# Kernel optimization log

Measured on AMD Instinct MI355X. Metric: run time of the kernel, lower is better.

The kernel has to match this reference:

```python
import jax, jax.numpy as jnp
import numpy as np

N = 50000      # nodes
E = 800000     # directed edges (avg degree 16)
F_IN = 128     # in_channels
HID = 256      # hidden_channels
OUT = 40       # out_channels (classes)


def setup_inputs() -> dict:
    key = jax.random.key(0)
    ks = jax.random.split(key, 6)
    x = jax.random.normal(ks[0], (N, F_IN), dtype=jnp.float32)
    edge_index = jax.random.randint(ks[1], (2, E), 0, N, dtype=jnp.int32)
    W1 = jax.random.normal(ks[2], (F_IN, HID), dtype=jnp.float32) * (1.0 / np.sqrt(F_IN))
    b1 = jnp.zeros((HID,), jnp.float32)
    W2 = jax.random.normal(ks[3], (HID, HID), dtype=jnp.float32) * (1.0 / np.sqrt(HID))
    b2 = jnp.zeros((HID,), jnp.float32)
    Wc = jax.random.normal(ks[4], (HID, OUT), dtype=jnp.float32) * (1.0 / np.sqrt(HID))
    bc = jnp.zeros((OUT,), jnp.float32)
    return {"x": x, "W1": W1, "b1": b1, "W2": W2, "b2": b2,
            "Wc": Wc, "bc": bc, "edge_index": edge_index}


def _gcn_conv(x, W, b, src, dst, norm):
    # PyG GCNConv: linear transform, then normalized sparse aggregation, then bias.
    h = x @ W                                    # [N, H]
    msg = h[src] * norm[:, None]                 # [E+N, H] gather + scale
    agg = jax.ops.segment_sum(msg, dst, num_segments=N)  # scatter-add
    return agg + b


def reference(x, W1, b1, W2, b2, Wc, bc, edge_index):
    # add self-loops (GCNConv default add_self_loops=True)
    loops = jnp.arange(N, dtype=edge_index.dtype)
    src = jnp.concatenate([edge_index[0], loops])
    dst = jnp.concatenate([edge_index[1], loops])
    # symmetric normalization D^-1/2 A D^-1/2 (degree counted at dst)
    deg = jax.ops.segment_sum(jnp.ones_like(dst, dtype=jnp.float32), dst,
                              num_segments=N)
    dinv = jax.lax.rsqrt(jnp.maximum(deg, 1.0))  # deg >= 1 due to self-loops
    norm = dinv[src] * dinv[dst]                 # [E+N]
    # layer 1 + ReLU (dropout is identity in eval mode)
    h = jax.nn.relu(_gcn_conv(x, W1, b1, src, dst, norm))
    # layer 2 + ReLU
    h = jax.nn.relu(_gcn_conv(h, W2, b2, src, dst, norm))
    # dense classifier
    return h @ Wc + bc  # [N, OUT]
```

## Files before the change

kernel.cpp:

```cpp
#include <hip/hip_runtime.h>

#define NNODES 50000
#define NEDGES 800000
#define F_IN   128
#define HID    256
#define NOUT   40
#define NBLK_SCAN ((NNODES + 255) / 256)
#define NBLK_CAST 6250
#define NBLK_DEG  2048
#define NBLK_PREP 432
#define EDGE_CHUNK 3125
#define NODES_PER_G 6250

typedef __attribute__((ext_vector_type(8))) _Float16 f16x8;
typedef __attribute__((ext_vector_type(4))) float f32x4;
typedef __attribute__((ext_vector_type(4))) unsigned short u16x4;
typedef __attribute__((ext_vector_type(8))) unsigned short u16x8;

__device__ __forceinline__ unsigned short f2h(float f) {
  return __builtin_bit_cast(unsigned short, (_Float16)f);
}
__device__ __forceinline__ float h2f(unsigned short u) {
  return (float)__builtin_bit_cast(_Float16, u);
}


__global__ __launch_bounds__(256) void k_pre(const float* __restrict__ X,
                                             unsigned short* __restrict__ Xh,
                                             const int* __restrict__ dst,
                                             int* __restrict__ count,
                                             const float* __restrict__ W1,
                                             const float* __restrict__ W2,
                                             const float* __restrict__ Wc,
                                             unsigned short* __restrict__ T1,
                                             unsigned short* __restrict__ T2,
                                             unsigned short* __restrict__ Tc) {
  int b = blockIdx.x, t = threadIdx.x;
  if (b < NBLK_CAST) {
    int i = b * 256 + t;
    float4 v = *reinterpret_cast<const float4*>(X + (size_t)i * 4);
    ushort4 o;
    o.x = f2h(v.x); o.y = f2h(v.y); o.z = f2h(v.z); o.w = f2h(v.w);
    *reinterpret_cast<ushort4*>(Xh + (size_t)i * 4) = o;
  } else if (b < NBLK_CAST + NBLK_DEG) {
    int db = b - NBLK_CAST;
    int g = b & 7;
    int chunk = db >> 3;
    int lo = g * NODES_PER_G, hi = lo + NODES_PER_G;
    int base = chunk * EDGE_CHUNK;
    for (int i = base + t; i < base + EDGE_CHUNK; i += 256) {
      int d = dst[i];
      if (d >= lo && d < hi) atomicAdd(&count[d], 1);
    }
  } else {
    int pb = b - NBLK_CAST - NBLK_DEG;
    if (pb < 128) {
      int idx = pb * 256 + t;
      int n = idx >> 7, k = idx & 127;
      T1[idx] = f2h(W1[(size_t)k * HID + n]);
    } else if (pb < 384) {
      int idx = (pb - 128) * 256 + t;
      int n = idx >> 8, k = idx & 255;
      T2[idx] = f2h(W2[(size_t)k * HID + n]);
    } else {
      int idx = (pb - 384) * 256 + t;
      int n = idx >> 8, k = idx & 255;
      float v = (n < NOUT) ? Wc[(size_t)k * NOUT + n] : 0.f;
      Tc[idx] = f2h(v);
    }
  }
}


__global__ __launch_bounds__(256) void k_scan1(const int* __restrict__ count,
                                               int* __restrict__ rowstart,
                                               int* __restrict__ bsum,
                                               float* __restrict__ dinv,
                                               int* __restrict__ boff,
                                               int* __restrict__ done) {
  __shared__ int tmp[256];
  __shared__ int lastFlag;
  int t = threadIdx.x;
  int i = blockIdx.x * 256 + t;
  int v = (i < NNODES) ? count[i] : 0;
  if (i < NNODES) dinv[i] = rsqrtf((float)(v + 1));
  tmp[t] = v;
  __syncthreads();
  for (int off = 1; off < 256; off <<= 1) {
    int x = (t >= off) ? tmp[t - off] : 0;
    __syncthreads();
    tmp[t] += x;
    __syncthreads();
  }
  if (i < NNODES) rowstart[i] = tmp[t] - v;
  if (t == 255) {
    bsum[blockIdx.x] = tmp[255];
    __threadfence();
  }
  __syncthreads();
  if (t == 0) lastFlag = (atomicAdd(done, 1) == (int)gridDim.x - 1);
  __syncthreads();
  if (lastFlag) {
    __threadfence();
    int v2 = (t < NBLK_SCAN) ? bsum[t] : 0;
    tmp[t] = v2;
    __syncthreads();
    for (int off = 1; off < 256; off <<= 1) {
      int x2 = (t >= off) ? tmp[t - off] : 0;
      __syncthreads();
      tmp[t] += x2;
      __syncthreads();
    }
    if (t < NBLK_SCAN) boff[t] = tmp[t] - v2;
  }
}


__global__ __launch_bounds__(256) void k_scatter(const int* __restrict__ src,
                                                 const int* __restrict__ dst,
                                                 const int* __restrict__ rowstart,
                                                 const int* __restrict__ boff,
                                                 int* __restrict__ cursor,
                                                 int* __restrict__ csr) {
  int g = blockIdx.x & 7;
  int chunk = blockIdx.x >> 3;
  int lo = g * NODES_PER_G, hi = lo + NODES_PER_G;
  int base = chunk * EDGE_CHUNK;
  for (int i = base + threadIdx.x; i < base + EDGE_CHUNK; i += 256) {
    int d = dst[i];
    if (d >= lo && d < hi) {
      int p = rowstart[d] + boff[d >> 8] + atomicAdd(&cursor[d], 1);
      csr[p] = src[i];
    }
  }
}


__global__ __launch_bounds__(256) void k_agg1(const unsigned short* __restrict__ X,
                                              const int* __restrict__ rowstart,
                                              const int* __restrict__ boff,
                                              const int* __restrict__ csr,
                                              const float* __restrict__ dinv,
                                              uint2* __restrict__ Y) {
  int wave = threadIdx.x >> 6, lane = threadIdx.x & 63;
  int node = blockIdx.x * 4 + wave;
  if (node >= NNODES) return;
  int half = lane >> 5, l32 = lane & 31;
  float di = dinv[node];
  float a[4] = {0.f, 0.f, 0.f, 0.f};
  int e = rowstart[node] + boff[node >> 8];
  int end = (node + 1 < NNODES) ? rowstart[node + 1] + boff[(node + 1) >> 8] : NEDGES;
  for (; e + 8 <= end; e += 8) {
    int s0 = csr[e + 0 + half], s1 = csr[e + 2 + half];
    int s2 = csr[e + 4 + half], s3 = csr[e + 6 + half];
    float w0 = dinv[s0] * di, w1 = dinv[s1] * di;
    float w2 = dinv[s2] * di, w3 = dinv[s3] * di;
    u16x4 r0 = *reinterpret_cast<const u16x4*>(X + (size_t)s0 * F_IN + l32 * 4);
    u16x4 r1 = *reinterpret_cast<const u16x4*>(X + (size_t)s1 * F_IN + l32 * 4);
    u16x4 r2 = *reinterpret_cast<const u16x4*>(X + (size_t)s2 * F_IN + l32 * 4);
    u16x4 r3 = *reinterpret_cast<const u16x4*>(X + (size_t)s3 * F_IN + l32 * 4);
#pragma unroll
    for (int k = 0; k < 4; k++) {
      a[k] = fmaf(h2f(r0[k]), w0, a[k]);
      a[k] = fmaf(h2f(r1[k]), w1, a[k]);
      a[k] = fmaf(h2f(r2[k]), w2, a[k]);
      a[k] = fmaf(h2f(r3[k]), w3, a[k]);
    }
  }
  for (; e + 2 <= end; e += 2) {
    int s = csr[e + half];
    float w = dinv[s] * di;
    u16x4 r = *reinterpret_cast<const u16x4*>(X + (size_t)s * F_IN + l32 * 4);
#pragma unroll
    for (int k = 0; k < 4; k++) a[k] = fmaf(h2f(r[k]), w, a[k]);
  }
  if (e < end) {
    int s = csr[e];
    float w = half ? 0.f : dinv[s] * di;
    u16x4 r = *reinterpret_cast<const u16x4*>(X + (size_t)s * F_IN + l32 * 4);
#pragma unroll
    for (int k = 0; k < 4; k++) a[k] = fmaf(h2f(r[k]), w, a[k]);
  }
#pragma unroll
  for (int k = 0; k < 4; k++) a[k] += __shfl_xor(a[k], 32);
  if (half == 0) {
    u16x4 self = *reinterpret_cast<const u16x4*>(X + (size_t)node * F_IN + l32 * 4);
    float dd = di * di;
#pragma unroll
    for (int k = 0; k < 4; k++) a[k] = fmaf(h2f(self[k]), dd, a[k]);
    uint2 o;
    o.x = (unsigned)f2h(a[0]) | ((unsigned)f2h(a[1]) << 16);
    o.y = (unsigned)f2h(a[2]) | ((unsigned)f2h(a[3]) << 16);
    Y[(size_t)node * 32 + l32] = o;
  }
}


__global__ __launch_bounds__(256) void k_agg2(const unsigned short* __restrict__ H,
                                              const int* __restrict__ rowstart,
                                              const int* __restrict__ boff,
                                              const int* __restrict__ csr,
                                              const float* __restrict__ dinv,
                                              uint4* __restrict__ Y) {
  int wave = threadIdx.x >> 6, lane = threadIdx.x & 63;
  int node = blockIdx.x * 4 + wave;
  if (node >= NNODES) return;
  int half = lane >> 5, l32 = lane & 31;
  float di = dinv[node];
  float a[8] = {0.f, 0.f, 0.f, 0.f, 0.f, 0.f, 0.f, 0.f};
  int e = rowstart[node] + boff[node >> 8];
  int end = (node + 1 < NNODES) ? rowstart[node + 1] + boff[(node + 1) >> 8] : NEDGES;
  for (; e + 8 <= end; e += 8) {
    int s0 = csr[e + 0 + half], s1 = csr[e + 2 + half];
    int s2 = csr[e + 4 + half], s3 = csr[e + 6 + half];
    float w0 = dinv[s0] * di, w1 = dinv[s1] * di;
    float w2 = dinv[s2] * di, w3 = dinv[s3] * di;
    u16x8 r0 = *reinterpret_cast<const u16x8*>(H + (size_t)s0 * HID + l32 * 8);
    u16x8 r1 = *reinterpret_cast<const u16x8*>(H + (size_t)s1 * HID + l32 * 8);
    u16x8 r2 = *reinterpret_cast<const u16x8*>(H + (size_t)s2 * HID + l32 * 8);
    u16x8 r3 = *reinterpret_cast<const u16x8*>(H + (size_t)s3 * HID + l32 * 8);
#pragma unroll
    for (int k = 0; k < 8; k++) {
      a[k] = fmaf(h2f(r0[k]), w0, a[k]);
      a[k] = fmaf(h2f(r1[k]), w1, a[k]);
      a[k] = fmaf(h2f(r2[k]), w2, a[k]);
      a[k] = fmaf(h2f(r3[k]), w3, a[k]);
    }
  }
  for (; e + 2 <= end; e += 2) {
    int s = csr[e + half];
    float w = dinv[s] * di;
    u16x8 r = *reinterpret_cast<const u16x8*>(H + (size_t)s * HID + l32 * 8);
#pragma unroll
    for (int k = 0; k < 8; k++) a[k] = fmaf(h2f(r[k]), w, a[k]);
  }
  if (e < end) {
    int s = csr[e];
    float w = half ? 0.f : dinv[s] * di;
    u16x8 r = *reinterpret_cast<const u16x8*>(H + (size_t)s * HID + l32 * 8);
#pragma unroll
    for (int k = 0; k < 8; k++) a[k] = fmaf(h2f(r[k]), w, a[k]);
  }
#pragma unroll
  for (int k = 0; k < 8; k++) a[k] += __shfl_xor(a[k], 32);
  if (half == 0) {
    u16x8 self = *reinterpret_cast<const u16x8*>(H + (size_t)node * HID + l32 * 8);
    float dd = di * di;
#pragma unroll
    for (int k = 0; k < 8; k++) a[k] = fmaf(h2f(self[k]), dd, a[k]);
    uint4 o;
    o.x = (unsigned)f2h(a[0]) | ((unsigned)f2h(a[1]) << 16);
    o.y = (unsigned)f2h(a[2]) | ((unsigned)f2h(a[3]) << 16);
    o.z = (unsigned)f2h(a[4]) | ((unsigned)f2h(a[5]) << 16);
    o.w = (unsigned)f2h(a[6]) | ((unsigned)f2h(a[7]) << 16);
    Y[(size_t)node * 32 + l32] = o;
  }
}


__global__ __launch_bounds__(256) void k_mgemm(const unsigned short* __restrict__ Ag,
                                               const unsigned short* __restrict__ Btg,
                                               const float* __restrict__ bias,
                                               unsigned short* __restrict__ Cout,
                                               int M, int Nc, int K) {
  __shared__ unsigned short Ah[2][128 * 40];
  __shared__ unsigned short Bh[2][128 * 40];
  int tid = threadIdx.x;
  int lane = tid & 63, w = tid >> 6;
  int wr = w >> 1, wc = w & 1;
  int bm = blockIdx.x * 128, bn = blockIdx.y * 128;
  int l15 = lane & 15, kg = lane >> 4;
  int row0 = tid >> 2, kq0 = (tid & 3) * 8;
  int gm0 = bm + row0, gm1 = bm + row0 + 64;

  f32x4 zero = {0.f, 0.f, 0.f, 0.f};
  f32x4 acc[4][4];
#pragma unroll
  for (int i = 0; i < 4; i++)
#pragma unroll
    for (int j = 0; j < 4; j++) acc[i][j] = zero;

  uint4 ra0, ra1, rb0, rb1;
  const uint4 z4 = {0, 0, 0, 0};
#define LOADT(KT)                                                                    \
  {                                                                                  \
    ra0 = z4; ra1 = z4;                                                              \
    if (gm0 < M) ra0 = *reinterpret_cast<const uint4*>(Ag + (size_t)gm0 * K + (KT) + kq0); \
    if (gm1 < M) ra1 = *reinterpret_cast<const uint4*>(Ag + (size_t)gm1 * K + (KT) + kq0); \
    rb0 = *reinterpret_cast<const uint4*>(Btg + (size_t)(bn + row0) * K + (KT) + kq0);     \
    rb1 = *reinterpret_cast<const uint4*>(Btg + (size_t)(bn + row0 + 64) * K + (KT) + kq0);\
  }
#define STORET(B)                                                       \
  {                                                                     \
    *reinterpret_cast<uint4*>(&Ah[B][row0 * 40 + kq0]) = ra0;           \
    *reinterpret_cast<uint4*>(&Ah[B][(row0 + 64) * 40 + kq0]) = ra1;    \
    *reinterpret_cast<uint4*>(&Bh[B][row0 * 40 + kq0]) = rb0;           \
    *reinterpret_cast<uint4*>(&Bh[B][(row0 + 64) * 40 + kq0]) = rb1;    \
  }

  LOADT(0);
  STORET(0);
  __syncthreads();
  int nt = K >> 5, cur = 0;
  for (int t = 0; t < nt; t++) {
    bool pf = (t + 1 < nt);
    if (pf) LOADT((t + 1) << 5);
    f16x8 fa[4], fb[4];
#pragma unroll
    for (int f = 0; f < 4; f++) {
      fa[f] = *reinterpret_cast<const f16x8*>(&Ah[cur][(wr * 64 + f * 16 + l15) * 40 + kg * 8]);
      fb[f] = *reinterpret_cast<const f16x8*>(&Bh[cur][(wc * 64 + f * 16 + l15) * 40 + kg * 8]);
    }
#pragma unroll
    for (int i = 0; i < 4; i++)
#pragma unroll
      for (int j = 0; j < 4; j++)
        acc[i][j] = __builtin_amdgcn_mfma_f32_16x16x32_f16(fa[i], fb[j], acc[i][j], 0, 0, 0);
    if (pf) STORET(cur ^ 1);
    __syncthreads();
    cur ^= 1;
  }
#undef LOADT
#undef STORET

  int r0 = kg * 4;
#pragma unroll
  for (int i = 0; i < 4; i++) {
    int gmBase = bm + wr * 64 + i * 16 + r0;
#pragma unroll
    for (int r = 0; r < 4; r++) {
      int gm = gmBase + r;
      if (gm >= M) continue;
#pragma unroll
      for (int j = 0; j < 4; j++) {
        int gn = bn + wc * 64 + j * 16 + l15;
        float v = acc[i][j][r] + bias[gn];
        v = fmaxf(v, 0.f);
        Cout[(size_t)gm * Nc + gn] = f2h(v);
      }
    }
  }
}


__global__ __launch_bounds__(256) void k_g2cls(const unsigned short* __restrict__ Ag,
                                               const unsigned short* __restrict__ W2t,
                                               const float* __restrict__ b2,
                                               const unsigned short* __restrict__ Wct,
                                               const float* __restrict__ bc,
                                               float* __restrict__ out, int M) {
  __shared__ unsigned short Ah[128 * 40];
  __shared__ unsigned short Bh[128 * 40];
  __shared__ unsigned short H2[128 * 136];
  __shared__ unsigned short WcS[48 * 40];
  int tid = threadIdx.x;
  int lane = tid & 63, w = tid >> 6;
  int wr = w >> 1, wc = w & 1;
  int bm = blockIdx.x * 128;
  int l15 = lane & 15, kg = lane >> 4;
  int row0 = tid >> 2, kq0 = (tid & 3) * 8;
  int gm0 = bm + row0, gm1 = bm + row0 + 64;

  f32x4 zero = {0.f, 0.f, 0.f, 0.f};
  f32x4 clsacc[2][3];
#pragma unroll
  for (int f = 0; f < 2; f++)
#pragma unroll
    for (int j = 0; j < 3; j++) clsacc[f][j] = zero;

  for (int halfN = 0; halfN < 2; halfN++) {
    f32x4 acc[4][4];
#pragma unroll
    for (int i = 0; i < 4; i++)
#pragma unroll
      for (int j = 0; j < 4; j++) acc[i][j] = zero;
    int bn = halfN * 128;
    for (int kt = 0; kt < HID; kt += 32) {
      uint4 ra0 = {0, 0, 0, 0}, ra1 = {0, 0, 0, 0};
      if (gm0 < M) ra0 = *reinterpret_cast<const uint4*>(Ag + (size_t)gm0 * HID + kt + kq0);
      if (gm1 < M) ra1 = *reinterpret_cast<const uint4*>(Ag + (size_t)gm1 * HID + kt + kq0);
      uint4 rb0 = *reinterpret_cast<const uint4*>(W2t + (size_t)(bn + row0) * HID + kt + kq0);
      uint4 rb1 = *reinterpret_cast<const uint4*>(W2t + (size_t)(bn + row0 + 64) * HID + kt + kq0);
      *reinterpret_cast<uint4*>(&Ah[row0 * 40 + kq0]) = ra0;
      *reinterpret_cast<uint4*>(&Ah[(row0 + 64) * 40 + kq0]) = ra1;
      *reinterpret_cast<uint4*>(&Bh[row0 * 40 + kq0]) = rb0;
      *reinterpret_cast<uint4*>(&Bh[(row0 + 64) * 40 + kq0]) = rb1;
      __syncthreads();
      f16x8 fa[4], fb[4];
#pragma unroll
      for (int f = 0; f < 4; f++) {
        fa[f] = *reinterpret_cast<const f16x8*>(&Ah[(wr * 64 + f * 16 + l15) * 40 + kg * 8]);
        fb[f] = *reinterpret_cast<const f16x8*>(&Bh[(wc * 64 + f * 16 + l15) * 40 + kg * 8]);
      }
#pragma unroll
      for (int i = 0; i < 4; i++)
#pragma unroll
        for (int j = 0; j < 4; j++)
          acc[i][j] = __builtin_amdgcn_mfma_f32_16x16x32_f16(fa[i], fb[j], acc[i][j], 0, 0, 0);
      __syncthreads();
    }
    int r0 = kg * 4;
#pragma unroll
    for (int i = 0; i < 4; i++)
#pragma unroll
      for (int r = 0; r < 4; r++) {
        int lrow = wr * 64 + i * 16 + r0 + r;
#pragma unroll
        for (int j = 0; j < 4; j++) {
          int lcol = wc * 64 + j * 16 + l15;
          float v = acc[i][j][r] + b2[bn + lcol];
          H2[lrow * 136 + lcol] = f2h(fmaxf(v, 0.f));
        }
      }
    __syncthreads();
    for (int kt2 = 0; kt2 < 128; kt2 += 32) {
      if (tid < 192) {
        int row = tid >> 2, kq = (tid & 3) * 8;
        *reinterpret_cast<uint4*>(&WcS[row * 40 + kq]) =
            *reinterpret_cast<const uint4*>(Wct + (size_t)row * HID + halfN * 128 + kt2 + kq);
      }
      __syncthreads();
      f16x8 fa[2], fb[3];
#pragma unroll
      for (int f = 0; f < 2; f++)
        fa[f] = *reinterpret_cast<const f16x8*>(&H2[(w * 32 + f * 16 + l15) * 136 + kt2 + kg * 8]);
#pragma unroll
      for (int j = 0; j < 3; j++)
        fb[j] = *reinterpret_cast<const f16x8*>(&WcS[(j * 16 + l15) * 40 + kg * 8]);
#pragma unroll
      for (int f = 0; f < 2; f++)
#pragma unroll
        for (int j = 0; j < 3; j++)
          clsacc[f][j] = __builtin_amdgcn_mfma_f32_16x16x32_f16(fa[f], fb[j], clsacc[f][j], 0, 0, 0);
      __syncthreads();
    }
  }
  int r0 = kg * 4;
#pragma unroll
  for (int f = 0; f < 2; f++) {
    int gmBase = bm + w * 32 + f * 16 + r0;
#pragma unroll
    for (int r = 0; r < 4; r++) {
      int gm = gmBase + r;
      if (gm >= M) continue;
#pragma unroll
      for (int j = 0; j < 3; j++) {
        int gn = j * 16 + l15;
        if (gn >= NOUT) continue;
        out[(size_t)gm * NOUT + gn] = clsacc[f][j][r] + bc[gn];
      }
    }
  }
}


extern "C" void kernel_launch(void* const* d_in, const int* in_sizes, int n_in,
                              void* d_out, int out_size, void* d_ws, size_t ws_size,
                              hipStream_t stream) {
  (void)in_sizes; (void)n_in; (void)out_size; (void)ws_size;
  const float* x  = (const float*)d_in[0];
  const float* W1 = (const float*)d_in[1];
  const float* b1 = (const float*)d_in[2];
  const float* W2 = (const float*)d_in[3];
  const float* b2 = (const float*)d_in[4];
  const float* Wc = (const float*)d_in[5];
  const float* bc = (const float*)d_in[6];
  const int* edge = (const int*)d_in[7];
  const int* srcE = edge;
  const int* dstE = edge + NEDGES;
  float* out = (float*)d_out;

  char* ws = (char*)d_ws;
  int*   count    = (int*)(ws + 0);
  int*   cursor   = (int*)(ws + 200064);
  int*   done     = (int*)(ws + 400064);
  int*   rowstart = (int*)(ws + 400128);
  float* dinv     = (float*)(ws + 600320);
  int*   csr      = (int*)(ws + 800384);
  int*   bsum     = (int*)(ws + 4000512);
  int*   boff     = (int*)(ws + 4001536);
  unsigned short* W1t = (unsigned short*)(ws + 4002560);
  unsigned short* W2t = (unsigned short*)(ws + 4068096);
  unsigned short* Wct = (unsigned short*)(ws + 4199168);
  unsigned short* xh  = (unsigned short*)(ws + 4264704);
  unsigned short* aggx = (unsigned short*)(ws + 17064704);
  unsigned short* h1   = (unsigned short*)(ws + 29864704);
  unsigned short* aggh = (unsigned short*)(ws + 55464704);

  hipMemsetAsync(ws, 0, 400128, stream);

  k_pre<<<NBLK_CAST + NBLK_DEG + NBLK_PREP, 256, 0, stream>>>(
      x, xh, dstE, count, W1, W2, Wc, W1t, W2t, Wct);
  k_scan1<<<NBLK_SCAN, 256, 0, stream>>>(count, rowstart, bsum, dinv, boff, done);
  k_scatter<<<NBLK_DEG, 256, 0, stream>>>(srcE, dstE, rowstart, boff, cursor, csr);

  k_agg1<<<(NNODES + 3) / 4, 256, 0, stream>>>(xh, rowstart, boff, csr, dinv, (uint2*)aggx);
  {
    dim3 grid((NNODES + 127) / 128, HID / 128);
    k_mgemm<<<grid, 256, 0, stream>>>(aggx, W1t, b1, h1, NNODES, HID, F_IN);
  }
  k_agg2<<<(NNODES + 3) / 4, 256, 0, stream>>>(h1, rowstart, boff, csr, dinv, (uint4*)aggh);
  k_g2cls<<<(NNODES + 127) / 128, 256, 0, stream>>>(aggh, W2t, b2, Wct, bc, out, NNODES);
}
```

Measured before the change: 308.7 us.

## Fuse CSR build stages into one cooperative kernel with grid syncs

Replaces the memset, preprocessing, scan and scatter launches with a single cooperative kernel of 2048 blocks. It zeroes the counters in-kernel, then separates the cast, degree count, block scan, offset scan and scatter phases with grid.sync(). The aim is to cut per-launch overhead and the memset. In exchange it needs 2048 co-resident blocks, which requires 8 blocks per CU at 256 threads, and each grid barrier has its own cost.

```diff
diff --git a/kernel.cpp b/kernel.cpp
--- a/kernel.cpp
+++ b/kernel.cpp
@@ -1,4 +1,7 @@
 #include <hip/hip_runtime.h>
+#include <hip/hip_cooperative_groups.h>
+
+namespace cg = cooperative_groups;
 
 #define NNODES 50000
 #define NEDGES 800000
@@ -7,10 +10,25 @@
 #define NOUT   40
 #define NBLK_SCAN ((NNODES + 255) / 256)
 #define NBLK_CAST 6250
-#define NBLK_DEG  2048
 #define NBLK_PREP 432
 #define EDGE_CHUNK 3125
 #define NODES_PER_G 6250
+#define CSR_BLOCKS 2048
+
+#define OFF_COUNT    0
+#define OFF_CURSOR   200064
+#define OFF_ROWSTART 400128
+#define OFF_DINV     600320
+#define OFF_CSR      800384
+#define OFF_BSUM     4000512
+#define OFF_BOFF     4001536
+#define OFF_W1T      4002560
+#define OFF_W2T      4068096
+#define OFF_WCT      4199168
+#define OFF_XH       4264704
+#define OFF_AGGX     17064704
+#define OFF_H1       29864704
+#define OFF_AGGH     55464704
 
 typedef __attribute__((ext_vector_type(8))) _Float16 f16x8;
 typedef __attribute__((ext_vector_type(4))) float f32x4;
@@ -25,112 +43,110 @@
 }
 
 
-__global__ __launch_bounds__(256) void k_pre(const float* __restrict__ X,
-                                             unsigned short* __restrict__ Xh,
-                                             const int* __restrict__ dst,
-                                             int* __restrict__ count,
-                                             const float* __restrict__ W1,
-                                             const float* __restrict__ W2,
-                                             const float* __restrict__ Wc,
-                                             unsigned short* __restrict__ T1,
-                                             unsigned short* __restrict__ T2,
-                                             unsigned short* __restrict__ Tc) {
+__global__ __launch_bounds__(256, 8) void k_csr(const float* __restrict__ X,
+                                                const int* __restrict__ srcE,
+                                                const int* __restrict__ dstE,
+                                                const float* __restrict__ W1,
+                                                const float* __restrict__ W2,
+                                                const float* __restrict__ Wc,
+                                                char* __restrict__ ws) {
+  cg::grid_group grid = cg::this_grid();
   int b = blockIdx.x, t = threadIdx.x;
-  if (b < NBLK_CAST) {
-    int i = b * 256 + t;
-    float4 v = *reinterpret_cast<const float4*>(X + (size_t)i * 4);
-    ushort4 o;
-    o.x = f2h(v.x); o.y = f2h(v.y); o.z = f2h(v.z); o.w = f2h(v.w);
-    *reinterpret_cast<ushort4*>(Xh + (size_t)i * 4) = o;
-  } else if (b < NBLK_CAST + NBLK_DEG) {
-    int db = b - NBLK_CAST;
-    int g = b & 7;
-    int chunk = db >> 3;
+  int* count    = (int*)(ws + OFF_COUNT);
+  int* cursor   = (int*)(ws + OFF_CURSOR);
+  int* rowstart = (int*)(ws + OFF_ROWSTART);
+  float* dinv   = (float*)(ws + OFF_DINV);
+  int* csr      = (int*)(ws + OFF_CSR);
+  int* bsum     = (int*)(ws + OFF_BSUM);
+  int* boff     = (int*)(ws + OFF_BOFF);
+  unsigned short* T1 = (unsigned short*)(ws + OFF_W1T);
+  unsigned short* T2 = (unsigned short*)(ws + OFF_W2T);
+  unsigned short* Tc = (unsigned short*)(ws + OFF_WCT);
+  unsigned short* Xh = (unsigned short*)(ws + OFF_XH);
+  (void)cursor;
+
+  {
+    int gi = b * 256 + t;
+    if (gi < 100032) ((int*)ws)[gi] = 0;
+    for (int c = b; c < NBLK_CAST; c += CSR_BLOCKS) {
+      int i = c * 256 + t;
+      float4 v = *reinterpret_cast<const float4*>(X + (size_t)i * 4);
+      ushort4 o;
+      o.x = f2h(v.x); o.y = f2h(v.y); o.z = f2h(v.z); o.w = f2h(v.w);
+      *reinterpret_cast<ushort4*>(Xh + (size_t)i * 4) = o;
+    }
+    for (int c = b; c < NBLK_PREP; c += CSR_BLOCKS) {
+      if (c < 128) {
+        int idx = c * 256 + t;
+        int n = idx >> 7, k = idx & 127;
+        T1[idx] = f2h(W1[(size_t)k * HID + n]);
+      } else if (c < 384) {
+        int idx = (c - 128) * 256 + t;
+        int n = idx >> 8, k = idx & 255;
+        T2[idx] = f2h(W2[(size_t)k * HID + n]);
+      } else {
+        int idx = (c - 384) * 256 + t;
+        int n = idx >> 8, k = idx & 255;
+        float v = (n < NOUT) ? Wc[(size_t)k * NOUT + n] : 0.f;
+        Tc[idx] = f2h(v);
+      }
+    }
+  }
+  grid.sync();
+
+  {
+    int g = b & 7, chunk = b >> 3;
     int lo = g * NODES_PER_G, hi = lo + NODES_PER_G;
     int base = chunk * EDGE_CHUNK;
     for (int i = base + t; i < base + EDGE_CHUNK; i += 256) {
-      int d = dst[i];
+      int d = dstE[i];
       if (d >= lo && d < hi) atomicAdd(&count[d], 1);
     }
-  } else {
-    int pb = b - NBLK_CAST - NBLK_DEG;
-    if (pb < 128) {
-      int idx = pb * 256 + t;
-      int n = idx >> 7, k = idx & 127;
-      T1[idx] = f2h(W1[(size_t)k * HID + n]);
-    } else if (pb < 384) {
-      int idx = (pb - 128) * 256 + t;
-      int n = idx >> 8, k = idx & 255;
-      T2[idx] = f2h(W2[(size_t)k * HID + n]);
-    } else {
-      int idx = (pb - 384) * 256 + t;
-      int n = idx >> 8, k = idx & 255;
-      float v = (n < NOUT) ? Wc[(size_t)k * NOUT + n] : 0.f;
-      Tc[idx] = f2h(v);
-    }
-  }
-}
-
-
-__global__ __launch_bounds__(256) void k_scan1(const int* __restrict__ count,
-                                               int* __restrict__ rowstart,
-                                               int* __restrict__ bsum,
-                                               float* __restrict__ dinv,
-                                               int* __restrict__ boff,
-                                               int* __restrict__ done) {
+  }
+  grid.sync();
+
   __shared__ int tmp[256];
-  __shared__ int lastFlag;
-  int t = threadIdx.x;
-  int i = blockIdx.x * 256 + t;
-  int v = (i < NNODES) ? count[i] : 0;
-  if (i < NNODES) dinv[i] = rsqrtf((float)(v + 1));
-  tmp[t] = v;
-  __syncthreads();
-  for (int off = 1; off < 256; off <<= 1) {
-    int x = (t >= off) ? tmp[t - off] : 0;
-    __syncthreads();
-    tmp[t] += x;
-    __syncthreads();
-  }
-  if (i < NNODES) rowstart[i] = tmp[t] - v;
-  if (t == 255) {
-    bsum[blockIdx.x] = tmp[255];
-    __threadfence();
-  }
-  __syncthreads();
-  if (t == 0) lastFlag = (atomicAdd(done, 1) == (int)gridDim.x - 1);
-  __syncthreads();
-  if (lastFlag) {
-    __threadfence();
-    int v2 = (t < NBLK_SCAN) ? bsum[t] : 0;
-    tmp[t] = v2;
+  if (b < NBLK_SCAN) {
+    int i = b * 256 + t;
+    int v = (i < NNODES) ? count[i] : 0;
+    if (i < NNODES) dinv[i] = rsqrtf((float)(v + 1));
+    tmp[t] = v;
     __syncthreads();
     for (int off = 1; off < 256; off <<= 1) {
-      int x2 = (t >= off) ? tmp[t - off] : 0;
-      __syncthreads();
-      tmp[t] += x2;
-      __syncthreads();
-    }
-    if (t < NBLK_SCAN) boff[t] = tmp[t] - v2;
-  }
-}
-
-
-__global__ __launch_bounds__(256) void k_scatter(const int* __restrict__ src,
-                                                 const int* __restrict__ dst,
-                                                 const int* __restrict__ rowstart,
-                                                 const int* __restrict__ boff,
-                                                 int* __restrict__ cursor,
-                                                 int* __restrict__ csr) {
-  int g = blockIdx.x & 7;
-  int chunk = blockIdx.x >> 3;
-  int lo = g * NODES_PER_G, hi = lo + NODES_PER_G;
-  int base = chunk * EDGE_CHUNK;
-  for (int i = base + threadIdx.x; i < base + EDGE_CHUNK; i += 256) {
-    int d = dst[i];
-    if (d >= lo && d < hi) {
-      int p = rowstart[d] + boff[d >> 8] + atomicAdd(&cursor[d], 1);
-      csr[p] = src[i];
+      int x = (t >= off) ? tmp[t - off] : 0;
+      __syncthreads();
+      tmp[t] += x;
+      __syncthreads();
+    }
+    if (i < NNODES) rowstart[i] = tmp[t] - v;
+    if (t == 255) bsum[b] = tmp[255];
+  }
+  grid.sync();
+
+  if (b == 0) {
+    int v = (t < NBLK_SCAN) ? bsum[t] : 0;
+    tmp[t] = v;
+    __syncthreads();
+    for (int off = 1; off < 256; off <<= 1) {
+      int x = (t >= off) ? tmp[t - off] : 0;
+      __syncthreads();
+      tmp[t] += x;
+      __syncthreads();
+    }
+    if (t < NBLK_SCAN) boff[t] = tmp[t] - v;
+  }
+  grid.sync();
+
+  {
+    int g = b & 7, chunk = b >> 3;
+    int lo = g * NODES_PER_G, hi = lo + NODES_PER_G;
+    int base = chunk * EDGE_CHUNK;
+    for (int i = base + t; i < base + EDGE_CHUNK; i += 256) {
+      int d = dstE[i];
+      if (d >= lo && d < hi) {
+        int p = rowstart[d] + boff[d >> 8] + atomicAdd(&cursor[d], 1);
+        csr[p] = srcE[i];
+      }
     }
   }
 }
@@ -471,28 +487,24 @@
   float* out = (float*)d_out;
 
   char* ws = (char*)d_ws;
-  int*   count    = (int*)(ws + 0);
-  int*   cursor   = (int*)(ws + 200064);
-  int*   done     = (int*)(ws + 400064);
-  int*   rowstart = (int*)(ws + 400128);
-  float* dinv     = (float*)(ws + 600320);
-  int*   csr      = (int*)(ws + 800384);
-  int*   bsum     = (int*)(ws + 4000512);
-  int*   boff     = (int*)(ws + 4001536);
-  unsigned short* W1t = (unsigned short*)(ws + 4002560);
-  unsigned short* W2t = (unsigned short*)(ws + 4068096);
-  unsigned short* Wct = (unsigned short*)(ws + 4199168);
-  unsigned short* xh  = (unsigned short*)(ws + 4264704);
-  unsigned short* aggx = (unsigned short*)(ws + 17064704);
-  unsigned short* h1   = (unsigned short*)(ws + 29864704);
-  unsigned short* aggh = (unsigned short*)(ws + 55464704);
-
-  hipMemsetAsync(ws, 0, 400128, stream);
-
-  k_pre<<<NBLK_CAST + NBLK_DEG + NBLK_PREP, 256, 0, stream>>>(
-      x, xh, dstE, count, W1, W2, Wc, W1t, W2t, Wct);
-  k_scan1<<<NBLK_SCAN, 256, 0, stream>>>(count, rowstart, bsum, dinv, boff, done);
-  k_scatter<<<NBLK_DEG, 256, 0, stream>>>(srcE, dstE, rowstart, boff, cursor, csr);
+  int*   rowstart = (int*)(ws + OFF_ROWSTART);
+  float* dinv     = (float*)(ws + OFF_DINV);
+  int*   csr      = (int*)(ws + OFF_CSR);
+  int*   boff     = (int*)(ws + OFF_BOFF);
+  unsigned short* W1t  = (unsigned short*)(ws + OFF_W1T);
+  unsigned short* W2t  = (unsigned short*)(ws + OFF_W2T);
+  unsigned short* Wct  = (unsigned short*)(ws + OFF_WCT);
+  unsigned short* xh   = (unsigned short*)(ws + OFF_XH);
+  unsigned short* aggx = (unsigned short*)(ws + OFF_AGGX);
+  unsigned short* h1   = (unsigned short*)(ws + OFF_H1);
+  unsigned short* aggh = (unsigned short*)(ws + OFF_AGGH);
+
+  {
+    void* args[] = {(void*)&x, (void*)&srcE, (void*)&dstE,
+                    (void*)&W1, (void*)&W2, (void*)&Wc, (void*)&ws};
+    hipLaunchCooperativeKernel((const void*)k_csr, dim3(CSR_BLOCKS), dim3(256),
+                               args, 0, stream);
+  }
 
   k_agg1<<<(NNODES + 3) / 4, 256, 0, stream>>>(xh, rowstart, boff, csr, dinv, (uint2*)aggx);
   {
```

Measured after the change: 1.069 ms. 246% more time.
